# Optimization experiments

Hardware: AMD Instinct MI355X
Metric: run time of the kernel (lower is better)

Reference implementation:

```python
import jax, jax.numpy as jnp
import numpy as np

SCALE = 30.0
MARGIN = 0.4
H = 0.333
NUM_CLASSES = 100000
EMB = 512
BATCH = 512


def setup_inputs() -> dict:
    key = jax.random.key(0)
    k1, k2, k3 = jax.random.split(key, 3)
    embeddings = jax.random.normal(k1, (BATCH, EMB), dtype=jnp.float32)
    labels = jax.random.randint(k2, (BATCH,), 0, NUM_CLASSES, dtype=jnp.int64)
    # xavier_uniform: bound = sqrt(6 / (fan_in + fan_out)) with fan_in=EMB, fan_out=NUM_CLASSES
    bound = float(np.sqrt(6.0 / (EMB + NUM_CLASSES)))
    weight = jax.random.uniform(k3, (NUM_CLASSES, EMB), dtype=jnp.float32, minval=-bound, maxval=bound)
    return {"embeddings": embeddings, "labels": labels, "weight": weight}


def reference(embeddings, labels, weight):
    n = embeddings.shape[0]
    rows = jnp.arange(n)

    emb_norm = jnp.linalg.norm(embeddings, axis=1, keepdims=True)      # [N,1]
    w_unit = weight / jnp.linalg.norm(weight, axis=1, keepdims=True)   # [C,D]
    emb_unit = embeddings / emb_norm                                   # [N,D]
    cosine = emb_unit @ w_unit.T                                       # [N,C]

    batch_mean = jnp.mean(emb_norm)
    batch_std = jnp.std(emb_norm, ddof=1)  # torch.std is unbiased
    margin_scaler = jnp.clip((emb_norm - batch_mean) / (batch_std + H), -1.0, 1.0)  # [N,1]
    adaptive_margin = MARGIN * (1.0 + margin_scaler[:, 0])             # [N]

    # Apply angular margin only at the label position (equivalent to the
    # one_hot scatter + where in the original, without a second N x C pass).
    cos_t = cosine[rows, labels]                                       # [N]
    cos_t_m = jnp.cos(jnp.arccos(cos_t) + adaptive_margin)             # [N]
    logits = SCALE * cosine.at[rows, labels].set(cos_t_m)              # [N,C]

    # cross-entropy with mean reduction
    lse = jax.nn.logsumexp(logits, axis=1)                             # [N]
    loss = jnp.mean(lse - logits[rows, labels])
    return loss
```

## Files before the change

kernel.cpp:

```cpp
#include <hip/hip_runtime.h>
#include <hip/hip_bf16.h>

#define C_NUM 100000
#define D_EMB 512
#define N_BATCH 512
#define SCALE_F 30.0f
#define MARGIN_F 0.4f
#define H_F 0.333f
#define NT2 782
#define PST 784
#define NCH 16

typedef __attribute__((ext_vector_type(8))) short bf16x8;
typedef __attribute__((ext_vector_type(4))) short bf16x4;
typedef __attribute__((ext_vector_type(4))) float f32x4;
typedef __attribute__((ext_vector_type(16))) float f32x16;

static __device__ __forceinline__ short f2bf(float f) {
  __hip_bfloat16 h = __float2bfloat16(f);
  union { __hip_bfloat16 b; short s; } u;
  u.b = h;
  return u.s;
}

static __device__ __forceinline__ float sq4(f32x4 v) {
  return v[0]*v[0] + v[1]*v[1] + v[2]*v[2] + v[3]*v[3];
}

static __device__ __forceinline__ void gload16(const void* g, void* l) {
  __builtin_amdgcn_global_load_lds(
      (const __attribute__((address_space(1))) void*)g,
      (__attribute__((address_space(3))) void*)l, 16, 0, 0);
}

__global__ __launch_bounds__(64) void k_rownorm(const float* __restrict__ emb,
                                                short* __restrict__ Aunit,
                                                float* __restrict__ norms) {
  const int i = blockIdx.x;
  const int l = threadIdx.x;
  const f32x4* row = reinterpret_cast<const f32x4*>(emb + (size_t)i * D_EMB);
  f32x4 v0 = row[l];
  f32x4 v1 = row[l + 64];
  float ss = sq4(v0) + sq4(v1);
#pragma unroll
  for (int m = 1; m < 64; m <<= 1) ss += __shfl_xor(ss, m);
  float nrm = sqrtf(ss);
  float inv = 1.0f / nrm;
  bf16x4 o0, o1;
#pragma unroll
  for (int q = 0; q < 4; ++q) { o0[q] = f2bf(v0[q] * inv); o1[q] = f2bf(v1[q] * inv); }
  bf16x4* dst = reinterpret_cast<bf16x4*>(Aunit + (size_t)i * D_EMB);
  dst[l] = o0;
  dst[l + 64] = o1;
  if (l == 0) norms[i] = nrm;
}

__global__ __launch_bounds__(512) void k_stats(const float* __restrict__ norms,
                                               float* __restrict__ marg) {
  __shared__ float red[8];
  const int t = threadIdx.x;
  const int lane = t & 63, wid = t >> 6;
  float x = norms[t];
  float s = x;
#pragma unroll
  for (int m = 1; m < 64; m <<= 1) s += __shfl_xor(s, m);
  if (lane == 0) red[wid] = s;
  __syncthreads();
  float tot = 0.f;
#pragma unroll
  for (int q = 0; q < 8; ++q) tot += red[q];
  const float mean = tot / 512.f;
  __syncthreads();
  float d = x - mean;
  float s2 = d * d;
#pragma unroll
  for (int m = 1; m < 64; m <<= 1) s2 += __shfl_xor(s2, m);
  if (lane == 0) red[wid] = s2;
  __syncthreads();
  float tot2 = 0.f;
#pragma unroll
  for (int q = 0; q < 8; ++q) tot2 += red[q];
  const float stdv = sqrtf(tot2 / 511.f);
  float msc = (x - mean) / (stdv + H_F);
  msc = fminf(1.f, fmaxf(-1.f, msc));
  marg[t] = MARGIN_F * (1.f + msc);
}

__global__ __launch_bounds__(256, 3) void k_main(const short* __restrict__ Aunit,
                                                 const float* __restrict__ weight,
                                                 const int* __restrict__ labels,
                                                 const float* __restrict__ marg,
                                                 float* __restrict__ partial,
                                                 float* __restrict__ tlogit) {
  __shared__ alignas(16) char As[2][8192];
  __shared__ alignas(16) char Ws[2][10240];
  __shared__ float winv[128];

  const int bid = blockIdx.x;
  const int grp = bid >> 5, within = bid & 31;
  const int rt = (within >> 3) & 3;
  const int ct = grp * 8 + (within & 7);
  if (ct >= NT2) return;

  const int tid = threadIdx.x;
  const int w = tid >> 6, lane = tid & 63;
  const int l31 = lane & 31, lhi = lane >> 5;

  const int ar0 = w * 32 + (lane >> 2);
  const int ak0 = ((lane & 3) * 16) ^ (((ar0 >> 1) & 3) << 4);
  const char* gAb0 = (const char*)Aunit + (size_t)(rt * 128 + ar0) * 1024 + ak0;
  const char* gAb1 = gAb0 + (size_t)16 * 1024;

  const int sc8 = tid >> 3;
  const int su  = tid & 7;
  const float* wbase0; const float* wbase1; const float* wbase2; const float* wbase3;
  int wdst0, wdst1, wdst2, wdst3;
  {
    int c0 = 0 * 32 + sc8, c1 = 1 * 32 + sc8, c2 = 2 * 32 + sc8, c3 = 3 * 32 + sc8;
    int g0 = ct * 128 + c0; if (g0 > C_NUM - 1) g0 = C_NUM - 1;
    int g1 = ct * 128 + c1; if (g1 > C_NUM - 1) g1 = C_NUM - 1;
    int g2 = ct * 128 + c2; if (g2 > C_NUM - 1) g2 = C_NUM - 1;
    int g3 = ct * 128 + c3; if (g3 > C_NUM - 1) g3 = C_NUM - 1;
    wbase0 = weight + (size_t)g0 * D_EMB + su * 4;
    wbase1 = weight + (size_t)g1 * D_EMB + su * 4;
    wbase2 = weight + (size_t)g2 * D_EMB + su * 4;
    wbase3 = weight + (size_t)g3 * D_EMB + su * 4;
    wdst0 = c0 * 80 + su * 8; wdst1 = c1 * 80 + su * 8;
    wdst2 = c2 * 80 + su * 8; wdst3 = c3 * 80 + su * 8;
  }

  const int xa = ((l31 >> 1) & 3) << 4;
  const int abase = (w * 32 + l31) * 64;

  f32x16 acc0, acc1, acc2, acc3;
#pragma unroll
  for (int q = 0; q < 16; ++q) { acc0[q] = 0.f; acc1[q] = 0.f; acc2[q] = 0.f; acc3[q] = 0.f; }
  float ssq0 = 0.f, ssq1 = 0.f, ssq2 = 0.f, ssq3 = 0.f;

  f32x4 pa0, pa1, pa2, pa3;
  f32x4 pb0, pb1, pb2, pb3;

#define WLOAD(R0,R1,R2,R3,OFF) { \
    R0 = *(const f32x4*)(wbase0 + (OFF)); R1 = *(const f32x4*)(wbase1 + (OFF)); \
    R2 = *(const f32x4*)(wbase2 + (OFF)); R3 = *(const f32x4*)(wbase3 + (OFF)); }

#define WWRITE(BUF,R0,R1,R2,R3) { \
    bf16x4 t0, t1, t2, t3; \
    _Pragma("unroll") \
    for (int e = 0; e < 4; ++e) { t0[e] = f2bf(R0[e]); t1[e] = f2bf(R1[e]); \
                                  t2[e] = f2bf(R2[e]); t3[e] = f2bf(R3[e]); } \
    *(bf16x4*)(&Ws[BUF][wdst0]) = t0; *(bf16x4*)(&Ws[BUF][wdst1]) = t1; \
    *(bf16x4*)(&Ws[BUF][wdst2]) = t2; *(bf16x4*)(&Ws[BUF][wdst3]) = t3; }

#define SSQADD(R0,R1,R2,R3) { ssq0 += sq4(R0); ssq1 += sq4(R1); \
                              ssq2 += sq4(R2); ssq3 += sq4(R3); }

#define COMPUTE(BUF) { \
    const char* Ab = As[BUF]; const char* Wb = Ws[BUF]; \
    __builtin_amdgcn_s_setprio(1); \
    _Pragma("unroll") \
    for (int kk = 0; kk < 2; ++kk) { \
      const int kb = kk * 32 + lhi * 16; \
      bf16x8 a  = *(const bf16x8*)(Ab + abase + (kb ^ xa)); \
      bf16x8 b0 = *(const bf16x8*)(Wb + (l31)      * 80 + kb); \
      bf16x8 b1 = *(const bf16x8*)(Wb + (32 + l31) * 80 + kb); \
      bf16x8 b2 = *(const bf16x8*)(Wb + (64 + l31) * 80 + kb); \
      bf16x8 b3 = *(const bf16x8*)(Wb + (96 + l31) * 80 + kb); \
      acc0 = __builtin_amdgcn_mfma_f32_32x32x16_bf16(a, b0, acc0, 0, 0, 0); \
      acc1 = __builtin_amdgcn_mfma_f32_32x32x16_bf16(a, b1, acc1, 0, 0, 0); \
      acc2 = __builtin_amdgcn_mfma_f32_32x32x16_bf16(a, b2, acc2, 0, 0, 0); \
      acc3 = __builtin_amdgcn_mfma_f32_32x32x16_bf16(a, b3, acc3, 0, 0, 0); \
    } \
    __builtin_amdgcn_s_setprio(0); }

  WLOAD(pa0, pa1, pa2, pa3, 0);
  __builtin_amdgcn_sched_barrier(0);
  gload16(gAb0, &As[0][w * 2048]);
  gload16(gAb1, &As[0][w * 2048 + 1024]);
  __builtin_amdgcn_sched_barrier(0);
  WLOAD(pb0, pb1, pb2, pb3, 32);
  __builtin_amdgcn_sched_barrier(0);
  asm volatile("s_waitcnt vmcnt(4)" ::: "memory");
  SSQADD(pa0, pa1, pa2, pa3);
  WWRITE(0, pa0, pa1, pa2, pa3);
  asm volatile("s_waitcnt lgkmcnt(0)" ::: "memory");
  __builtin_amdgcn_s_barrier();
  __builtin_amdgcn_sched_barrier(0);

  for (int i = 0; i < 8; ++i) {
    {
      const int ao = (2 * i + 1) * 64;
      gload16(gAb0 + ao, &As[1][w * 2048]);
      gload16(gAb1 + ao, &As[1][w * 2048 + 1024]);
      __builtin_amdgcn_sched_barrier(0);
      int cw = 2 * i + 2; if (cw > 15) cw = 15;
      WLOAD(pa0, pa1, pa2, pa3, cw * 32);
      __builtin_amdgcn_sched_barrier(0);
      COMPUTE(0);
      asm volatile("s_waitcnt vmcnt(4)" ::: "memory");
      SSQADD(pb0, pb1, pb2, pb3);
      WWRITE(1, pb0, pb1, pb2, pb3);
      asm volatile("s_waitcnt lgkmcnt(0)" ::: "memory");
      __builtin_amdgcn_s_barrier();
      __builtin_amdgcn_sched_barrier(0);
    }
    {
      int ca = 2 * i + 2; if (ca > 15) ca = 15;
      const int ao = ca * 64;
      gload16(gAb0 + ao, &As[0][w * 2048]);
      gload16(gAb1 + ao, &As[0][w * 2048 + 1024]);
      __builtin_amdgcn_sched_barrier(0);
      int cw = 2 * i + 3; if (cw > 15) cw = 15;
      WLOAD(pb0, pb1, pb2, pb3, cw * 32);
      __builtin_amdgcn_sched_barrier(0);
      COMPUTE(1);
      asm volatile("s_waitcnt vmcnt(4)" ::: "memory");
      if (2 * i + 2 <= 15) SSQADD(pa0, pa1, pa2, pa3);
      WWRITE(0, pa0, pa1, pa2, pa3);
      asm volatile("s_waitcnt lgkmcnt(0)" ::: "memory");
      __builtin_amdgcn_s_barrier();
      __builtin_amdgcn_sched_barrier(0);
    }
  }

  {
    float s0 = ssq0, s1 = ssq1, s2 = ssq2, s3 = ssq3;
#pragma unroll
    for (int m = 1; m < 8; m <<= 1) {
      s0 += __shfl_xor(s0, m); s1 += __shfl_xor(s1, m);
      s2 += __shfl_xor(s2, m); s3 += __shfl_xor(s3, m);
    }
    if (su == 0) {
      winv[sc8]      = (s0 > 0.f) ? rsqrtf(s0) : 0.f;
      winv[32 + sc8] = (s1 > 0.f) ? rsqrtf(s1) : 0.f;
      winv[64 + sc8] = (s2 > 0.f) ? rsqrtf(s2) : 0.f;
      winv[96 + sc8] = (s3 > 0.f) ? rsqrtf(s3) : 0.f;
    }
  }
  __syncthreads();

  const float wv0 = winv[l31];
  const float wv1 = winv[32 + l31];
  const float wv2 = winv[64 + l31];
  const float wv3 = winv[96 + l31];
  const int cb = ct * 128;
#pragma unroll
  for (int r = 0; r < 16; ++r) {
    const int rowf = (r & 3) + 8 * (r >> 2) + 4 * lhi;
    const int R = rt * 128 + w * 32 + rowf;
    const int lab = labels[R];
    float v = 0.f;
#pragma unroll
    for (int ni = 0; ni < 4; ++ni) {
      const int gcc = cb + ni * 32 + l31;
      const float wv = (ni == 0) ? wv0 : (ni == 1) ? wv1 : (ni == 2) ? wv2 : wv3;
      const float av = (ni == 0) ? acc0[r] : (ni == 1) ? acc1[r] : (ni == 2) ? acc2[r] : acc3[r];
      const float cosv = av * wv;
      float lg = SCALE_F * cosv;
      if (lab == gcc) {
        float ctv = fminf(1.f, fmaxf(-1.f, cosv));
        float lt = SCALE_F * cosf(acosf(ctv) + marg[R]);
        lg = lt;
        tlogit[R] = lt;
      }
      v += (gcc < C_NUM) ? __expf(lg) : 0.f;
    }
    v += __shfl_xor(v, 1);
    v += __shfl_xor(v, 2);
    v += __shfl_xor(v, 4);
    v += __shfl_xor(v, 8);
    v += __shfl_xor(v, 16);
    if (l31 == 0) partial[(size_t)R * PST + ct] = v;
  }
#undef WLOAD
#undef WWRITE
#undef SSQADD
#undef COMPUTE
}

__global__ __launch_bounds__(64) void k_reduce(const float* __restrict__ partial,
                                               const float* __restrict__ tlogit,
                                               float* __restrict__ term) {
  const int r = blockIdx.x;
  const int l = threadIdx.x;
  const float* row = partial + (size_t)r * PST;
  float s = 0.f;
  for (int b = l; b < NT2; b += 64)
    s += row[b];
#pragma unroll
  for (int m = 1; m < 64; m <<= 1) s += __shfl_xor(s, m);
  if (l == 0) term[r] = logf(s) - tlogit[r];
}

__global__ __launch_bounds__(512) void k_final(const float* __restrict__ term,
                                               float* __restrict__ out) {
  __shared__ float red[8];
  const int t = threadIdx.x;
  const int lane = t & 63, wid = t >> 6;
  float v = term[t];
#pragma unroll
  for (int m = 1; m < 64; m <<= 1) v += __shfl_xor(v, m);
  if (lane == 0) red[wid] = v;
  __syncthreads();
  if (t == 0) {
    float tot = 0.f;
#pragma unroll
    for (int q = 0; q < 8; ++q) tot += red[q];
    out[0] = tot / 512.f;
  }
}

extern "C" void kernel_launch(void* const* d_in, const int* in_sizes, int n_in,
                              void* d_out, int out_size, void* d_ws, size_t ws_size,
                              hipStream_t stream) {
  const float* emb    = (const float*)d_in[0];
  const int*   labels = (const int*)d_in[1];
  const float* weight = (const float*)d_in[2];
  float* out = (float*)d_out;

  char* ws = (char*)d_ws;
  short* Aunit   = (short*)ws;
  float* norms   = (float*)(ws + 524288);
  float* marg    = (float*)(ws + 524288 + 2048);
  float* tlog    = (float*)(ws + 524288 + 4096);
  float* term    = (float*)(ws + 524288 + 6144);
  float* partial = (float*)(ws + 524288 + 8192);

  k_rownorm<<<N_BATCH, 64, 0, stream>>>(emb, Aunit, norms);
  k_stats<<<1, 512, 0, stream>>>(norms, marg);
  k_main<<<98 * 32, 256, 0, stream>>>(Aunit, weight, labels, marg, partial, tlog);
  k_reduce<<<N_BATCH, 64, 0, stream>>>(partial, tlog, term);
  k_final<<<1, 512, 0, stream>>>(term, out);
}
```

Before: 134.7 us.

## Double K-step per stage to 64 and prefetch weights two chunks ahead

Widens each pipeline stage from a K-chunk of 32 to 64, which halves the number of barrier-synchronised iterations. Weight rows are now prefetched two 32-wide chunks ahead in registers, and A tiles are loaded with a new swizzle and a 128-byte row stride. LDS per block grows to about 69KB, up from about 37KB. That may cut occupancy below the launch_bounds target of 3 blocks per CU, and more weight prefetch registers stay live.

After: 158.9 us. +17.9%, slower.

```diff
diff --git a/kernel.cpp b/kernel.cpp
--- a/kernel.cpp
+++ b/kernel.cpp
@@ -9,7 +9,6 @@
 #define H_F 0.333f
 #define NT2 782
 #define PST 784
-#define NCH 16
 
 typedef __attribute__((ext_vector_type(8))) short bf16x8;
 typedef __attribute__((ext_vector_type(4))) short bf16x4;
@@ -92,8 +91,8 @@
                                                  const float* __restrict__ marg,
                                                  float* __restrict__ partial,
                                                  float* __restrict__ tlogit) {
-  __shared__ alignas(16) char As[2][8192];
-  __shared__ alignas(16) char Ws[2][10240];
+  __shared__ alignas(16) char As[2][16384];
+  __shared__ alignas(16) char Ws[2][18432];
   __shared__ float winv[128];
 
   const int bid = blockIdx.x;
@@ -106,10 +105,9 @@
   const int w = tid >> 6, lane = tid & 63;
   const int l31 = lane & 31, lhi = lane >> 5;
 
-  const int ar0 = w * 32 + (lane >> 2);
-  const int ak0 = ((lane & 3) * 16) ^ (((ar0 >> 1) & 3) << 4);
-  const char* gAb0 = (const char*)Aunit + (size_t)(rt * 128 + ar0) * 1024 + ak0;
-  const char* gAb1 = gAb0 + (size_t)16 * 1024;
+  const int arr = w * 32 + (lane >> 3);
+  const int akbs = ((lane & 7) * 16) ^ ((arr & 7) << 4);
+  const char* gA = (const char*)Aunit + (size_t)(rt * 128 + arr) * 1024 + akbs;
 
   const int sc8 = tid >> 3;
   const int su  = tid & 7;
@@ -125,12 +123,16 @@
     wbase1 = weight + (size_t)g1 * D_EMB + su * 4;
     wbase2 = weight + (size_t)g2 * D_EMB + su * 4;
     wbase3 = weight + (size_t)g3 * D_EMB + su * 4;
-    wdst0 = c0 * 80 + su * 8; wdst1 = c1 * 80 + su * 8;
-    wdst2 = c2 * 80 + su * 8; wdst3 = c3 * 80 + su * 8;
-  }
-
-  const int xa = ((l31 >> 1) & 3) << 4;
-  const int abase = (w * 32 + l31) * 64;
+    wdst0 = c0 * 144 + su * 8; wdst1 = c1 * 144 + su * 8;
+    wdst2 = c2 * 144 + su * 8; wdst3 = c3 * 144 + su * 8;
+  }
+
+  const int xa = (l31 & 7) << 4;
+  const int abase = (w * 32 + l31) * 128;
+  const int bb0 = (l31)       * 144;
+  const int bb1 = (32 + l31)  * 144;
+  const int bb2 = (64 + l31)  * 144;
+  const int bb3 = (96 + l31)  * 144;
 
   f32x16 acc0, acc1, acc2, acc3;
 #pragma unroll
@@ -144,28 +146,31 @@
     R0 = *(const f32x4*)(wbase0 + (OFF)); R1 = *(const f32x4*)(wbase1 + (OFF)); \
     R2 = *(const f32x4*)(wbase2 + (OFF)); R3 = *(const f32x4*)(wbase3 + (OFF)); }
 
-#define WWRITE(BUF,R0,R1,R2,R3) { \
-    bf16x4 t0, t1, t2, t3; \
+#define WWRITE2(BUF) { \
+    bf16x4 t0, t1, t2, t3, u0, u1, u2, u3; \
     _Pragma("unroll") \
-    for (int e = 0; e < 4; ++e) { t0[e] = f2bf(R0[e]); t1[e] = f2bf(R1[e]); \
-                                  t2[e] = f2bf(R2[e]); t3[e] = f2bf(R3[e]); } \
+    for (int e = 0; e < 4; ++e) { \
+      t0[e] = f2bf(pa0[e]); t1[e] = f2bf(pa1[e]); t2[e] = f2bf(pa2[e]); t3[e] = f2bf(pa3[e]); \
+      u0[e] = f2bf(pb0[e]); u1[e] = f2bf(pb1[e]); u2[e] = f2bf(pb2[e]); u3[e] = f2bf(pb3[e]); } \
     *(bf16x4*)(&Ws[BUF][wdst0]) = t0; *(bf16x4*)(&Ws[BUF][wdst1]) = t1; \
-    *(bf16x4*)(&Ws[BUF][wdst2]) = t2; *(bf16x4*)(&Ws[BUF][wdst3]) = t3; }
-
-#define SSQADD(R0,R1,R2,R3) { ssq0 += sq4(R0); ssq1 += sq4(R1); \
-                              ssq2 += sq4(R2); ssq3 += sq4(R3); }
-
-#define COMPUTE(BUF) { \
+    *(bf16x4*)(&Ws[BUF][wdst2]) = t2; *(bf16x4*)(&Ws[BUF][wdst3]) = t3; \
+    *(bf16x4*)(&Ws[BUF][wdst0 + 64]) = u0; *(bf16x4*)(&Ws[BUF][wdst1 + 64]) = u1; \
+    *(bf16x4*)(&Ws[BUF][wdst2 + 64]) = u2; *(bf16x4*)(&Ws[BUF][wdst3 + 64]) = u3; }
+
+#define SSQADD2() { ssq0 += sq4(pa0) + sq4(pb0); ssq1 += sq4(pa1) + sq4(pb1); \
+                    ssq2 += sq4(pa2) + sq4(pb2); ssq3 += sq4(pa3) + sq4(pb3); }
+
+#define COMPUTE64(BUF) { \
     const char* Ab = As[BUF]; const char* Wb = Ws[BUF]; \
     __builtin_amdgcn_s_setprio(1); \
     _Pragma("unroll") \
-    for (int kk = 0; kk < 2; ++kk) { \
+    for (int kk = 0; kk < 4; ++kk) { \
       const int kb = kk * 32 + lhi * 16; \
       bf16x8 a  = *(const bf16x8*)(Ab + abase + (kb ^ xa)); \
-      bf16x8 b0 = *(const bf16x8*)(Wb + (l31)      * 80 + kb); \
-      bf16x8 b1 = *(const bf16x8*)(Wb + (32 + l31) * 80 + kb); \
-      bf16x8 b2 = *(const bf16x8*)(Wb + (64 + l31) * 80 + kb); \
-      bf16x8 b3 = *(const bf16x8*)(Wb + (96 + l31) * 80 + kb); \
+      bf16x8 b0 = *(const bf16x8*)(Wb + bb0 + kb); \
+      bf16x8 b1 = *(const bf16x8*)(Wb + bb1 + kb); \
+      bf16x8 b2 = *(const bf16x8*)(Wb + bb2 + kb); \
+      bf16x8 b3 = *(const bf16x8*)(Wb + bb3 + kb); \
       acc0 = __builtin_amdgcn_mfma_f32_32x32x16_bf16(a, b0, acc0, 0, 0, 0); \
       acc1 = __builtin_amdgcn_mfma_f32_32x32x16_bf16(a, b1, acc1, 0, 0, 0); \
       acc2 = __builtin_amdgcn_mfma_f32_32x32x16_bf16(a, b2, acc2, 0, 0, 0); \
@@ -174,53 +179,50 @@
     __builtin_amdgcn_s_setprio(0); }
 
   WLOAD(pa0, pa1, pa2, pa3, 0);
-  __builtin_amdgcn_sched_barrier(0);
-  gload16(gAb0, &As[0][w * 2048]);
-  gload16(gAb1, &As[0][w * 2048 + 1024]);
-  __builtin_amdgcn_sched_barrier(0);
   WLOAD(pb0, pb1, pb2, pb3, 32);
   __builtin_amdgcn_sched_barrier(0);
+#pragma unroll
+  for (int i = 0; i < 4; ++i)
+    gload16(gA + (size_t)i * 8192, &As[0][w * 4096 + i * 1024]);
+  __builtin_amdgcn_sched_barrier(0);
   asm volatile("s_waitcnt vmcnt(4)" ::: "memory");
-  SSQADD(pa0, pa1, pa2, pa3);
-  WWRITE(0, pa0, pa1, pa2, pa3);
+  SSQADD2();
+  WWRITE2(0);
+  __builtin_amdgcn_sched_barrier(0);
+  WLOAD(pa0, pa1, pa2, pa3, 2 * 32);
+  WLOAD(pb0, pb1, pb2, pb3, 3 * 32);
+  __builtin_amdgcn_sched_barrier(0);
+  asm volatile("s_waitcnt vmcnt(8)" ::: "memory");
   asm volatile("s_waitcnt lgkmcnt(0)" ::: "memory");
   __builtin_amdgcn_s_barrier();
   __builtin_amdgcn_sched_barrier(0);
 
-  for (int i = 0; i < 8; ++i) {
+  for (int p = 0; p < 8; ++p) {
+    const int buf = p & 1;
     {
-      const int ao = (2 * i + 1) * 64;
-      gload16(gAb0 + ao, &As[1][w * 2048]);
-      gload16(gAb1 + ao, &As[1][w * 2048 + 1024]);
-      __builtin_amdgcn_sched_barrier(0);
-      int cw = 2 * i + 2; if (cw > 15) cw = 15;
-      WLOAD(pa0, pa1, pa2, pa3, cw * 32);
-      __builtin_amdgcn_sched_barrier(0);
-      COMPUTE(0);
-      asm volatile("s_waitcnt vmcnt(4)" ::: "memory");
-      SSQADD(pb0, pb1, pb2, pb3);
-      WWRITE(1, pb0, pb1, pb2, pb3);
-      asm volatile("s_waitcnt lgkmcnt(0)" ::: "memory");
-      __builtin_amdgcn_s_barrier();
-      __builtin_amdgcn_sched_barrier(0);
-    }
+      const int ap = (p + 1 > 7) ? 7 : (p + 1);
+      const char* src = gA + ap * 128;
+#pragma unroll
+      for (int i = 0; i < 4; ++i)
+        gload16(src + (size_t)i * 8192, &As[buf ^ 1][w * 4096 + i * 1024]);
+    }
+    __builtin_amdgcn_sched_barrier(0);
+    COMPUTE64(buf);
+    asm volatile("s_waitcnt vmcnt(4)" ::: "memory");
+    if (p < 7) { SSQADD2(); }
+    WWRITE2(buf ^ 1);
+    __builtin_amdgcn_sched_barrier(0);
     {
-      int ca = 2 * i + 2; if (ca > 15) ca = 15;
-      const int ao = ca * 64;
-      gload16(gAb0 + ao, &As[0][w * 2048]);
-      gload16(gAb1 + ao, &As[0][w * 2048 + 1024]);
-      __builtin_amdgcn_sched_barrier(0);
-      int cw = 2 * i + 3; if (cw > 15) cw = 15;
-      WLOAD(pb0, pb1, pb2, pb3, cw * 32);
-      __builtin_amdgcn_sched_barrier(0);
-      COMPUTE(1);
-      asm volatile("s_waitcnt vmcnt(4)" ::: "memory");
-      if (2 * i + 2 <= 15) SSQADD(pa0, pa1, pa2, pa3);
-      WWRITE(0, pa0, pa1, pa2, pa3);
-      asm volatile("s_waitcnt lgkmcnt(0)" ::: "memory");
-      __builtin_amdgcn_s_barrier();
-      __builtin_amdgcn_sched_barrier(0);
-    }
+      int ce = 2 * p + 4; if (ce > 15) ce = 15;
+      int co = 2 * p + 5; if (co > 15) co = 15;
+      WLOAD(pa0, pa1, pa2, pa3, ce * 32);
+      WLOAD(pb0, pb1, pb2, pb3, co * 32);
+    }
+    __builtin_amdgcn_sched_barrier(0);
+    asm volatile("s_waitcnt vmcnt(8)" ::: "memory");
+    asm volatile("s_waitcnt lgkmcnt(0)" ::: "memory");
+    __builtin_amdgcn_s_barrier();
+    __builtin_amdgcn_sched_barrier(0);
   }
 
   {
@@ -273,9 +275,9 @@
     if (l31 == 0) partial[(size_t)R * PST + ct] = v;
   }
 #undef WLOAD
-#undef WWRITE
-#undef SSQADD
-#undef COMPUTE
+#undef WWRITE2
+#undef SSQADD2
+#undef COMPUTE64
 }
 
 __global__ __launch_bounds__(64) void k_reduce(const float* __restrict__ partial,
```
